# Kernel optimization log

Measured on AMD Instinct MI355X. Metric: run time of the kernel, lower is better.

The kernel has to match this reference:

```python
import jax, jax.numpy as jnp
import numpy as np
from jax import lax

N, B, H, E = 50, 1024, 256, 256
FEA, SF = 8, 5
C_TANH = 10.0  # tanh_exploration, use_tanh=True for pointer


def setup_inputs() -> dict:
    key = jax.random.key(0)
    ks = iter(jax.random.split(key, 40))
    def rn(shape):
        return jax.random.normal(next(ks), shape, dtype=jnp.float32)
    def up(shape):
        s = 1.0 / np.sqrt(shape[-1])
        return jax.random.uniform(next(ks), shape, minval=-s, maxval=s, dtype=jnp.float32)
    inp = {
        'start_fea': rn((B, SF)),
        'decoder_input': rn((B, E)),
        'embedded_inputs': rn((N, B, E)),
        'hidden_h': rn((B, H)),
        'hidden_c': rn((B, H)),
        'context': rn((N, B, H)),
        'V': rn((B, N, FEA)),
        'V_reach_mask': jnp.zeros((B, N), dtype=bool),
        # LSTMCell (pointer decoder)
        'lstm_w_ih': up((4 * H, E)), 'lstm_w_hh': up((4 * H, H)),
        'lstm_b_ih': up((4 * H,)), 'lstm_b_hh': up((4 * H,)),
        # pointer attention
        'ptr_wq': up((H, H)), 'ptr_bq': up((H,)),
        'ptr_wr': up((H, H)), 'ptr_br': up((H,)), 'ptr_v': up((H,)),
        # glimpse attention
        'glp_wq': up((H, H)), 'glp_bq': up((H,)),
        'glp_wr': up((H, H)), 'glp_br': up((H,)), 'glp_v': up((H,)),
        # eta branch
        'fn_w': up((H, SF)),
        'eta_w_ih': up((4 * H, H)), 'eta_w_hh': up((4 * H, H)),
        'eta_b_ih': up((4 * H,)), 'eta_b_hh': up((4 * H,)),
        'eta_lin_w': up((1, 2 * H)), 'eta_lin_b': up((1,)),
    }
    return inp


def _lstm_cell(x, h, c, wi, wh, bi, bh):
    z = x @ wi.T + bi + h @ wh.T + bh
    i, f, g, o = jnp.split(z, 4, axis=1)  # torch chunk order i,f,g,o
    c2 = jax.nn.sigmoid(f) * c + jax.nn.sigmoid(i) * jnp.tanh(g)
    return jax.nn.sigmoid(o) * jnp.tanh(c2), c2


def _mask_modify(m):
    # if a row is all True, un-mask its last column
    return m.at[:, -1].set(jnp.where(m.all(axis=1), False, m[:, -1]))


def reference(start_fea, decoder_input, embedded_inputs, hidden_h, hidden_c,
              context, V, V_reach_mask,
              lstm_w_ih, lstm_w_hh, lstm_b_ih, lstm_b_hh,
              ptr_wq, ptr_bq, ptr_wr, ptr_br, ptr_v,
              glp_wq, glp_bq, glp_wr, glp_br, glp_v,
              fn_w, eta_w_ih, eta_w_hh, eta_b_ih, eta_b_hh,
              eta_lin_w, eta_lin_b):
    n_steps, bsz = embedded_inputs.shape[0], embedded_inputs.shape[1]
    barange = jnp.arange(bsz)
    # project_ref is a 1x1 conv over fixed context -> precompute once: [B,H,N]
    e_ptr = jnp.einsum('nbh,gh->bgn', context, ptr_wr) + ptr_br[None, :, None]
    e_glp = jnp.einsum('nbh,gh->bgn', context, glp_wr) + glp_br[None, :, None]

    def attn_logits(q_in, e, wq, bq, v):
        q = q_in @ wq.T + bq  # [B,H]
        return jnp.einsum('h,bhn->bn', v, jnp.tanh(q[:, :, None] + e))

    first_node = start_fea @ fn_w.T  # [B,H], no bias
    he, ce = _lstm_cell(first_node, hidden_h, hidden_c, eta_w_ih, eta_w_hh, eta_b_ih, eta_b_hh)
    mask0 = _mask_modify(V_reach_mask)

    def step(carry, step_i):
        h, c, mask, idxs, dec_in, heh, cec, last_node, cur_eta = carry
        upd = _mask_modify(mask.at[barange, idxs].set(True))
        logit_mask = jnp.where(step_i == 0, mask, upd)
        # pointer LSTM step
        h, c = _lstm_cell(dec_in, h, c, lstm_w_ih, lstm_w_hh, lstm_b_ih, lstm_b_hh)
        g_l = h
        # one glimpse (n_glimpses=1, mask_glimpses=True, use_tanh=False)
        u = attn_logits(g_l, e_glp, glp_wq, glp_bq, glp_v)
        u = jnp.where(logit_mask, -jnp.inf, u)
        g_l = jnp.einsum('bhn,bn->bh', e_glp, jax.nn.softmax(u, axis=1))
        # pointer (use_tanh=True, C=10, mask_logits=True)
        u = attn_logits(g_l, e_ptr, ptr_wq, ptr_bq, ptr_v)
        logits = jnp.where(logit_mask, -jnp.inf, C_TANH * jnp.tanh(u))
        log_p = jax.nn.log_softmax(logits, axis=1)  # [B,N]
        new_idxs = jnp.argmax(log_p, axis=1)  # greedy decode
        # eta branch
        cur_node = context[new_idxs, barange]  # [B,H]
        heh, cec = _lstm_cell(cur_node, heh, cec, eta_w_ih, eta_w_hh, eta_b_ih, eta_b_hh)
        eta = jnp.concatenate([last_node, cur_node], axis=1) @ eta_lin_w.T + eta_lin_b  # [B,1]
        cur_eta = cur_eta + eta
        dec_in2 = embedded_inputs[new_idxs, barange]  # [B,E]
        new_carry = (h, c, logit_mask, new_idxs, dec_in2, heh, cec, cur_node, cur_eta)
        return new_carry, (log_p, new_idxs, cur_eta[:, 0])

    init = (hidden_h, hidden_c, mask0, jnp.zeros((bsz,), jnp.int32), decoder_input,
            he, ce, first_node, jnp.zeros((bsz, 1), jnp.float32))
    _, (log_ps, sels, etas) = lax.scan(step, init, jnp.arange(n_steps))
    # stack along step dim -> [B, N, ...]
    return log_ps.transpose(1, 0, 2), sels.T, etas.T
```

## Files before the change

kernel.cpp:

```cpp
#include <hip/hip_runtime.h>
#include <hip/hip_bf16.h>

#define NSTEP 50
#define BSZ   1024
#define HD    256
#define RPB   2
#define NEG_INF (-__builtin_inff())

#define OFF_SEL ((size_t)BSZ * NSTEP * NSTEP)
#define OFF_ETA (OFF_SEL + (size_t)BSZ * NSTEP)

__device__ __forceinline__ float sigf(float x)      { return 1.f / (1.f + __expf(-x)); }
__device__ __forceinline__ float tanh_fast(float x) { return 1.f - 2.f / (__expf(2.f * x) + 1.f); }

__device__ __forceinline__ float wave_sum(float v) {
#pragma unroll
  for (int o = 1; o < 64; o <<= 1) v += __shfl_xor(v, o);
  return v;
}
__device__ __forceinline__ float wave_max(float v) {
#pragma unroll
  for (int o = 1; o < 64; o <<= 1) v = fmaxf(v, __shfl_xor(v, o));
  return v;
}

__global__ __launch_bounds__(256) void init_kernel(
    const float* __restrict__ w_ih, const float* __restrict__ w_hh,
    const float* __restrict__ b_ih, const float* __restrict__ b_hh,
    const float* __restrict__ glp_wq, const float* __restrict__ ptr_wq,
    float* __restrict__ wT2, float* __restrict__ bc,
    float* __restrict__ wqTg, float* __restrict__ wqTp)
{
  const int bid = blockIdx.x, tid = threadIdx.x;
  if (bid < 512) {
    const int k = bid;
    const float* src = (k < 256) ? (w_ih + k) : (w_hh + (k - 256));
#pragma unroll
    for (int g = 0; g < 4; ++g)
      wT2[(size_t)k * 1024 + tid * 4 + g] = src[(size_t)(g * 256 + tid) * 256];
  } else if (bid < 516) {
    const int j = (bid - 512) * 256 + tid;
    bc[j] = b_ih[j] + b_hh[j];
  } else {
    const int k = bid - 516;
    wqTg[(size_t)k * 256 + tid] = glp_wq[(size_t)tid * 256 + k];
    wqTp[(size_t)k * 256 + tid] = ptr_wq[(size_t)tid * 256 + k];
  }
}

__global__ __launch_bounds__(256) void e_kernel(
    const float* __restrict__ context,
    const float* __restrict__ glp_wr, const float* __restrict__ glp_br,
    const float* __restrict__ ptr_wr, const float* __restrict__ ptr_br,
    float* __restrict__ e_glp, float* __restrict__ e_ptr)
{
  __shared__ float ctx_lds[32][256];
  const int tid = threadIdx.x;
  const int n   = blockIdx.x >> 5;
  const int b0  = (blockIdx.x & 31) << 5;
  const float* src = context + ((size_t)n * BSZ + b0) * HD;
  for (int i = tid; i < 32 * 64; i += 256) {
    const int row = i >> 6, k4 = (i & 63) << 2;
    *(float4*)&ctx_lds[row][k4] = *(const float4*)&src[row * HD + k4];
  }
  __syncthreads();
  const int g  = tid;
  const float bg = glp_br[g], bp = ptr_br[g];
  for (int rg = 0; rg < 2; ++rg) {
    float ag[16], ap[16];
#pragma unroll
    for (int i = 0; i < 16; ++i) { ag[i] = 0.f; ap[i] = 0.f; }
    for (int k = 0; k < 256; k += 4) {
      float4 wg = *(const float4*)&glp_wr[g * HD + k];
      float4 wp = *(const float4*)&ptr_wr[g * HD + k];
#pragma unroll
      for (int i = 0; i < 16; ++i) {
        float4 a = *(const float4*)&ctx_lds[rg * 16 + i][k];
        ag[i] += a.x * wg.x + a.y * wg.y + a.z * wg.z + a.w * wg.w;
        ap[i] += a.x * wp.x + a.y * wp.y + a.z * wp.z + a.w * wp.w;
      }
    }
#pragma unroll
    for (int i = 0; i < 16; ++i) {
      const int b = b0 + rg * 16 + i;
      e_glp[((size_t)b * NSTEP + n) * HD + g] = ag[i] + bg;
      e_ptr[((size_t)b * NSTEP + n) * HD + g] = ap[i] + bp;
    }
  }
}

__global__ __launch_bounds__(256) void zx_kernel(
    const float* __restrict__ embedded, const float* __restrict__ decoder_input,
    const float* __restrict__ wT2, float* __restrict__ zx)
{
  __shared__ float x_lds[32][256];
  const int tid = threadIdx.x;
  const int n   = blockIdx.x >> 5;
  const int b0  = (blockIdx.x & 31) << 5;
  const float* src = (n < NSTEP) ? (embedded + ((size_t)n * BSZ + b0) * HD)
                                 : (decoder_input + (size_t)b0 * HD);
  for (int i = tid; i < 32 * 64; i += 256) {
    const int row = i >> 6, k4 = (i & 63) << 2;
    *(float4*)&x_lds[row][k4] = *(const float4*)&src[row * HD + k4];
  }
  __syncthreads();
  const float* wp = wT2 + (tid << 2);
  for (int rg = 0; rg < 2; ++rg) {
    float4 acc[16];
#pragma unroll
    for (int i = 0; i < 16; ++i) acc[i] = make_float4(0.f, 0.f, 0.f, 0.f);
    for (int k = 0; k < 256; k += 4) {
      float4 w0 = *(const float4*)(wp + (size_t)(k + 0) * 1024);
      float4 w1 = *(const float4*)(wp + (size_t)(k + 1) * 1024);
      float4 w2 = *(const float4*)(wp + (size_t)(k + 2) * 1024);
      float4 w3 = *(const float4*)(wp + (size_t)(k + 3) * 1024);
#pragma unroll
      for (int i = 0; i < 16; ++i) {
        float4 a = *(const float4*)&x_lds[rg * 16 + i][k];
        acc[i].x += a.x * w0.x + a.y * w1.x + a.z * w2.x + a.w * w3.x;
        acc[i].y += a.x * w0.y + a.y * w1.y + a.z * w2.y + a.w * w3.y;
        acc[i].z += a.x * w0.z + a.y * w1.z + a.z * w2.z + a.w * w3.z;
        acc[i].w += a.x * w0.w + a.y * w1.w + a.z * w2.w + a.w * w3.w;
      }
    }
#pragma unroll
    for (int i = 0; i < 16; ++i)
      *(float4*)&zx[((size_t)n * BSZ + (b0 + rg * 16 + i)) * 1024 + (tid << 2)] = acc[i];
  }
}

template <int PRE>
__global__ __launch_bounds__(512, 4) void dec_kernel(
    const float* __restrict__ start_fea,
    const float* __restrict__ decoder_input,
    const float* __restrict__ embedded,
    const float* __restrict__ hidden_h,
    const float* __restrict__ hidden_c,
    const float* __restrict__ context,
    const unsigned char* __restrict__ vmask,
    const float* __restrict__ glp_bq, const float* __restrict__ glp_v,
    const float* __restrict__ ptr_bq, const float* __restrict__ ptr_v,
    const float* __restrict__ fn_w,
    const float* __restrict__ eta_lw, const float* __restrict__ eta_lb,
    const float* __restrict__ wT2, const float* __restrict__ bc,
    const float* __restrict__ wqTg, const float* __restrict__ wqTp,
    const float* __restrict__ e_glp, const float* __restrict__ e_ptr,
    const float* __restrict__ zx,
    float* __restrict__ out)
{
  __shared__ float a_lds[RPB][512];
  __shared__ float z_lds[RPB][1024];
  __shared__ float q_lds[RPB][512];
  __shared__ float u_lds[RPB][52];
  __shared__ unsigned char mask_lds[RPB][64];
  __shared__ float ms_lds[RPB][4][2];
  __shared__ int   idx_lds[RPB];
  __shared__ float red_lds[8];
  __shared__ float eta_lds[RPB];

  const int tid  = threadIdx.x;
  const int col  = tid & 255;
  const int hf   = tid >> 8;
  const int wav  = tid >> 6;
  const int lane = tid & 63;
  const int b0   = blockIdx.x * RPB;
  const int cr   = wav >> 2;
  const int cq   = wav & 3;
  const int n0   = cq * 13;
  const int n1   = (cq == 3) ? NSTEP : (n0 + 13);
  const int k0   = hf << 7;
  const int j2   = tid * 2;

  float c_reg, ln_reg;

  {
    const int r = hf, b = b0 + r;
    a_lds[r][256 + col] = hidden_h[(size_t)b * HD + col];
    if (!PRE) a_lds[r][col] = decoder_input[(size_t)b * HD + col];
    c_reg = hidden_c[(size_t)b * HD + col];
    float fn = 0.f;
#pragma unroll
    for (int k = 0; k < 5; ++k) fn += start_fea[b * 5 + k] * fn_w[col * 5 + k];
    ln_reg = fn;
  }
  if (tid < RPB * NSTEP) {
    const int r = tid / NSTEP, n = tid - r * NSTEP;
    mask_lds[r][n] = vmask[(size_t)(b0 + r) * NSTEP + n];
  }
  if (tid < RPB) { eta_lds[tid] = 0.f; idx_lds[tid] = NSTEP; }
  __syncthreads();
  if (tid < RPB) {
    bool all = true;
    for (int n = 0; n < NSTEP; ++n) all = all && (mask_lds[tid][n] != 0);
    if (all) mask_lds[tid][NSTEP - 1] = 0;
  }
  __syncthreads();

  const float bch0 = bc[col], bch1 = bc[col + 256], bch2 = bc[col + 512], bch3 = bc[col + 768];
  const float lw0 = eta_lw[col], lw1 = eta_lw[HD + col];
  const float etaB = eta_lb[0];
  const float4 v4g  = *(const float4*)&glp_v[lane << 2];
  const float4 v4p  = *(const float4*)&ptr_v[lane << 2];
  const float4 v4bg = *(const float4*)&glp_bq[lane << 2];
  const float4 v4bp = *(const float4*)&ptr_bq[lane << 2];

  for (int t = 0; t < NSTEP; ++t) {
    {
      float2 acc[RPB];
      if (PRE) {
#pragma unroll
        for (int i = 0; i < RPB; ++i)
          acc[i] = *(const float2*)&zx[((size_t)idx_lds[i] * BSZ + (b0 + i)) * 1024 + j2];
      } else {
#pragma unroll
        for (int i = 0; i < RPB; ++i) acc[i] = make_float2(0.f, 0.f);
      }
      const int K0 = PRE ? 256 : 0;
      for (int k = K0; k < 512; k += 4) {
        float4 a4[RPB];
#pragma unroll
        for (int i = 0; i < RPB; ++i) a4[i] = *(const float4*)&a_lds[i][k];
        const float2 w0 = *(const float2*)&wT2[(size_t)(k + 0) * 1024 + j2];
        const float2 w1 = *(const float2*)&wT2[(size_t)(k + 1) * 1024 + j2];
        const float2 w2 = *(const float2*)&wT2[(size_t)(k + 2) * 1024 + j2];
        const float2 w3 = *(const float2*)&wT2[(size_t)(k + 3) * 1024 + j2];
#pragma unroll
        for (int i = 0; i < RPB; ++i) {
          acc[i].x += a4[i].x * w0.x + a4[i].y * w1.x + a4[i].z * w2.x + a4[i].w * w3.x;
          acc[i].y += a4[i].x * w0.y + a4[i].y * w1.y + a4[i].z * w2.y + a4[i].w * w3.y;
        }
      }
#pragma unroll
      for (int i = 0; i < RPB; ++i) *(float2*)&z_lds[i][j2] = acc[i];
    }
    __syncthreads();
    {
      const float4 z4 = *(const float4*)&z_lds[hf][col << 2];
      const float zi = z4.x + bch0, zf = z4.y + bch1, zg = z4.z + bch2, zo = z4.w + bch3;
      const float cn = sigf(zf) * c_reg + sigf(zi) * tanh_fast(zg);
      c_reg = cn;
      a_lds[hf][256 + col] = sigf(zo) * tanh_fast(cn);
    }
    __syncthreads();
    {
      float accB[RPB] = {0.f, 0.f};
      for (int k = k0; k < k0 + 128; k += 4) {
        float4 a4[RPB];
#pragma unroll
        for (int i = 0; i < RPB; ++i) a4[i] = *(const float4*)&a_lds[i][256 + k];
        const float w0 = wqTg[(size_t)(k + 0) * 256 + col];
        const float w1 = wqTg[(size_t)(k + 1) * 256 + col];
        const float w2 = wqTg[(size_t)(k + 2) * 256 + col];
        const float w3 = wqTg[(size_t)(k + 3) * 256 + col];
#pragma unroll
        for (int i = 0; i < RPB; ++i)
          accB[i] += a4[i].x * w0 + a4[i].y * w1 + a4[i].z * w2 + a4[i].w * w3;
      }
#pragma unroll
      for (int i = 0; i < RPB; ++i) q_lds[i][(hf << 8) + col] = accB[i];
    }
    __syncthreads();
    {
      const int r = cr, b = b0 + r;
      float4 q4;
      {
        const float4 p0 = *(const float4*)&q_lds[r][lane << 2];
        const float4 p1 = *(const float4*)&q_lds[r][256 + (lane << 2)];
        q4 = make_float4(p0.x + p1.x + v4bg.x, p0.y + p1.y + v4bg.y,
                         p0.z + p1.z + v4bg.z, p0.w + p1.w + v4bg.w);
      }
      float m = NEG_INF, s = 0.f;
      float4 G = make_float4(0.f, 0.f, 0.f, 0.f);
      const float* eb = e_glp + (size_t)b * NSTEP * HD;
      for (int n = n0; n < n1; ++n) {
        if (mask_lds[r][n]) continue;
        const float4 e4 = *(const float4*)&eb[n * HD + (lane << 2)];
        float uu = v4g.x * tanh_fast(q4.x + e4.x) + v4g.y * tanh_fast(q4.y + e4.y)
                 + v4g.z * tanh_fast(q4.z + e4.z) + v4g.w * tanh_fast(q4.w + e4.w);
        uu = wave_sum(uu);
        if (uu > m) {
          const float sc = __expf(m - uu);
          s *= sc; G.x *= sc; G.y *= sc; G.z *= sc; G.w *= sc;
          m = uu;
        }
        const float p = __expf(uu - m);
        s += p;
        G.x += p * e4.x; G.y += p * e4.y; G.z += p * e4.z; G.w += p * e4.w;
      }
      if (lane == 0) { ms_lds[r][cq][0] = m; ms_lds[r][cq][1] = s; }
      __syncthreads();
      float mg = NEG_INF;
#pragma unroll
      for (int q = 0; q < 4; ++q) mg = fmaxf(mg, ms_lds[r][q][0]);
      float Z = 0.f;
#pragma unroll
      for (int q = 0; q < 4; ++q) Z += ms_lds[r][q][1] * __expf(ms_lds[r][q][0] - mg);
      const float sc = __expf(m - mg) / Z;
      G.x *= sc; G.y *= sc; G.z *= sc; G.w *= sc;
      *(float4*)&z_lds[r][(cq << 8) + (lane << 2)] = G;
    }
    __syncthreads();
    {
      float accE[RPB] = {0.f, 0.f};
      for (int k = k0; k < k0 + 128; k += 4) {
        float4 g4[RPB];
#pragma unroll
        for (int i = 0; i < RPB; ++i) {
          const float4 g0 = *(const float4*)&z_lds[i][k];
          const float4 g1 = *(const float4*)&z_lds[i][256 + k];
          const float4 g2 = *(const float4*)&z_lds[i][512 + k];
          const float4 g3 = *(const float4*)&z_lds[i][768 + k];
          g4[i] = make_float4(g0.x + g1.x + g2.x + g3.x, g0.y + g1.y + g2.y + g3.y,
                              g0.z + g1.z + g2.z + g3.z, g0.w + g1.w + g2.w + g3.w);
        }
        const float w0 = wqTp[(size_t)(k + 0) * 256 + col];
        const float w1 = wqTp[(size_t)(k + 1) * 256 + col];
        const float w2 = wqTp[(size_t)(k + 2) * 256 + col];
        const float w3 = wqTp[(size_t)(k + 3) * 256 + col];
#pragma unroll
        for (int i = 0; i < RPB; ++i)
          accE[i] += g4[i].x * w0 + g4[i].y * w1 + g4[i].z * w2 + g4[i].w * w3;
      }
#pragma unroll
      for (int i = 0; i < RPB; ++i) q_lds[i][(hf << 8) + col] = accE[i];
    }
    __syncthreads();
    {
      const int r = cr, b = b0 + r;
      float4 q4;
      {
        const float4 p0 = *(const float4*)&q_lds[r][lane << 2];
        const float4 p1 = *(const float4*)&q_lds[r][256 + (lane << 2)];
        q4 = make_float4(p0.x + p1.x + v4bp.x, p0.y + p1.y + v4bp.y,
                         p0.z + p1.z + v4bp.z, p0.w + p1.w + v4bp.w);
      }
      const float* eb = e_ptr + (size_t)b * NSTEP * HD;
      for (int n = n0; n < n1; ++n) {
        const float4 e4 = *(const float4*)&eb[n * HD + (lane << 2)];
        float uu = v4p.x * tanh_fast(q4.x + e4.x) + v4p.y * tanh_fast(q4.y + e4.y)
                 + v4p.z * tanh_fast(q4.z + e4.z) + v4p.w * tanh_fast(q4.w + e4.w);
        uu = wave_sum(uu);
        if (lane == 0) u_lds[r][n] = uu;
      }
    }
    __syncthreads();
    if (wav < RPB) {
      const int r = wav, b = b0 + r;
      const bool mk = (lane < NSTEP) ? (mask_lds[r][lane] != 0) : true;
      const float lg = mk ? NEG_INF : (10.f * tanh_fast(u_lds[r][lane]));
      const float m  = wave_max(lg);
      const float ex = (lane < NSTEP) ? __expf(lg - m) : 0.f;
      const float ss = wave_sum(ex);
      const float ls = __logf(ss);
      if (lane < NSTEP)
        out[(size_t)b * (NSTEP * NSTEP) + (size_t)t * NSTEP + lane] =
            mk ? -1.0e30f : ((lg - m) - ls);
      float av = lg;
      int   ai = lane;
#pragma unroll
      for (int o = 1; o < 64; o <<= 1) {
        const float ov = __shfl_xor(av, o);
        const int   oi = __shfl_xor(ai, o);
        if (ov > av || (ov == av && oi < ai)) { av = ov; ai = oi; }
      }
      if (lane == 0) {
        idx_lds[r] = ai;
        out[OFF_SEL + (size_t)b * NSTEP + t] = (float)ai;
      }
    }
    __syncthreads();
    {
      const int r = hf, b = b0 + r;
      const int ix = idx_lds[r];
      const float cur = context[((size_t)ix * BSZ + b) * HD + col];
      float pr = ln_reg * lw0 + cur * lw1;
      ln_reg = cur;
      if (!PRE) a_lds[r][col] = embedded[((size_t)ix * BSZ + b) * HD + col];
      pr = wave_sum(pr);
      if (lane == 0) red_lds[wav] = pr;
    }
    __syncthreads();
    if (tid < RPB) {
      const int r = tid;
      const float s = red_lds[r * 4 + 0] + red_lds[r * 4 + 1]
                    + red_lds[r * 4 + 2] + red_lds[r * 4 + 3];
      const float ev = eta_lds[r] + s + etaB;
      eta_lds[r] = ev;
      out[OFF_ETA + (size_t)(b0 + r) * NSTEP + t] = ev;
      const int ix = idx_lds[r];
      mask_lds[r][ix] = 1;
      bool all = true;
      for (int n = 0; n < NSTEP; ++n) all = all && (mask_lds[r][n] != 0);
      if (all) mask_lds[r][NSTEP - 1] = 0;
    }
    __syncthreads();
  }
}

extern "C" void kernel_launch(void* const* d_in, const int* in_sizes, int n_in,
                              void* d_out, int out_size, void* d_ws, size_t ws_size,
                              hipStream_t stream) {
  const float* start_fea  = (const float*)d_in[0];
  const float* decoder_in = (const float*)d_in[1];
  const float* embedded   = (const float*)d_in[2];
  const float* hidden_h   = (const float*)d_in[3];
  const float* hidden_c   = (const float*)d_in[4];
  const float* context    = (const float*)d_in[5];
  const unsigned char* vmask = (const unsigned char*)d_in[7];
  const float* lstm_w_ih  = (const float*)d_in[8];
  const float* lstm_w_hh  = (const float*)d_in[9];
  const float* lstm_b_ih  = (const float*)d_in[10];
  const float* lstm_b_hh  = (const float*)d_in[11];
  const float* ptr_wq     = (const float*)d_in[12];
  const float* ptr_bq     = (const float*)d_in[13];
  const float* ptr_wr     = (const float*)d_in[14];
  const float* ptr_br     = (const float*)d_in[15];
  const float* ptr_v      = (const float*)d_in[16];
  const float* glp_wq     = (const float*)d_in[17];
  const float* glp_bq     = (const float*)d_in[18];
  const float* glp_wr     = (const float*)d_in[19];
  const float* glp_br     = (const float*)d_in[20];
  const float* glp_v      = (const float*)d_in[21];
  const float* fn_w       = (const float*)d_in[22];
  const float* eta_lw     = (const float*)d_in[27];
  const float* eta_lb     = (const float*)d_in[28];

  float* ws    = (float*)d_ws;
  float* e_glp = ws;
  float* e_ptr = e_glp + (size_t)BSZ * NSTEP * HD;
  float* wT2   = e_ptr + (size_t)BSZ * NSTEP * HD;
  float* bc    = wT2 + (size_t)512 * 1024;
  float* wqTg  = bc + 1024;
  float* wqTp  = wqTg + 65536;
  float* zx    = wqTp + 65536;

  const size_t need_pre =
      ((size_t)BSZ * NSTEP * HD * 2 + (size_t)512 * 1024 + 1024 + 2 * 65536 +
       (size_t)(NSTEP + 1) * BSZ * 1024) * sizeof(float);
  const bool pre = (ws_size >= need_pre);

  init_kernel<<<772, 256, 0, stream>>>(lstm_w_ih, lstm_w_hh, lstm_b_ih, lstm_b_hh,
                                       glp_wq, ptr_wq, wT2, bc, wqTg, wqTp);
  e_kernel<<<NSTEP * 32, 256, 0, stream>>>(context, glp_wr, glp_br, ptr_wr, ptr_br, e_glp, e_ptr);
  if (pre) {
    zx_kernel<<<(NSTEP + 1) * 32, 256, 0, stream>>>(embedded, decoder_in, wT2, zx);
    dec_kernel<1><<<BSZ / RPB, 512, 0, stream>>>(
        start_fea, decoder_in, embedded, hidden_h, hidden_c, context, vmask,
        glp_bq, glp_v, ptr_bq, ptr_v, fn_w, eta_lw, eta_lb,
        wT2, bc, wqTg, wqTp, e_glp, e_ptr, zx, (float*)d_out);
  } else {
    dec_kernel<0><<<BSZ / RPB, 512, 0, stream>>>(
        start_fea, decoder_in, embedded, hidden_h, hidden_c, context, vmask,
        glp_bq, glp_v, ptr_bq, ptr_v, fn_w, eta_lw, eta_lb,
        wT2, bc, wqTg, wqTp, e_glp, e_ptr, zx, (float*)d_out);
  }
}
```

Measured before the change: 5.995 ms.

## Process four batch rows per 1024-thread block to halve weight re-reads

Doubles rows per block from 2 to 4 and block size from 512 to 1024 threads. Each thread now owns one gate column, and the query projections split K four ways, so every weight load from global memory serves four batch rows. The goal is to cut the L2/HBM traffic from re-streaming the LSTM and query weights on each step. It also skips masked nodes in the pointer attention loop. The cost is fewer blocks (256), an extra reduction pass through LDS with more barriers, and lower occupancy from dropping the launch-bounds hint.

```diff
diff --git a/kernel.cpp b/kernel.cpp
--- a/kernel.cpp
+++ b/kernel.cpp
@@ -4,7 +4,7 @@
 #define NSTEP 50
 #define BSZ   1024
 #define HD    256
-#define RPB   2
+#define RPB   4
 #define NEG_INF (-__builtin_inff())
 
 #define OFF_SEL ((size_t)BSZ * NSTEP * NSTEP)
@@ -130,7 +130,7 @@
 }
 
 template <int PRE>
-__global__ __launch_bounds__(512, 4) void dec_kernel(
+__global__ __launch_bounds__(1024) void dec_kernel(
     const float* __restrict__ start_fea,
     const float* __restrict__ decoder_input,
     const float* __restrict__ embedded,
@@ -150,17 +150,18 @@
 {
   __shared__ float a_lds[RPB][512];
   __shared__ float z_lds[RPB][1024];
-  __shared__ float q_lds[RPB][512];
+  __shared__ float z2_lds[RPB][1024];
+  __shared__ float qf_lds[RPB][256];
   __shared__ float u_lds[RPB][52];
   __shared__ unsigned char mask_lds[RPB][64];
   __shared__ float ms_lds[RPB][4][2];
   __shared__ int   idx_lds[RPB];
-  __shared__ float red_lds[8];
+  __shared__ float red_lds[16];
   __shared__ float eta_lds[RPB];
 
   const int tid  = threadIdx.x;
   const int col  = tid & 255;
-  const int hf   = tid >> 8;
+  const int rr   = tid >> 8;
   const int wav  = tid >> 6;
   const int lane = tid & 63;
   const int b0   = blockIdx.x * RPB;
@@ -168,15 +169,14 @@
   const int cq   = wav & 3;
   const int n0   = cq * 13;
   const int n1   = (cq == 3) ? NSTEP : (n0 + 13);
-  const int k0   = hf << 7;
-  const int j2   = tid * 2;
+  const int kq   = rr;
 
   float c_reg, ln_reg;
 
   {
-    const int r = hf, b = b0 + r;
-    a_lds[r][256 + col] = hidden_h[(size_t)b * HD + col];
-    if (!PRE) a_lds[r][col] = decoder_input[(size_t)b * HD + col];
+    const int b = b0 + rr;
+    a_lds[rr][256 + col] = hidden_h[(size_t)b * HD + col];
+    if (!PRE) a_lds[rr][col] = decoder_input[(size_t)b * HD + col];
     c_reg = hidden_c[(size_t)b * HD + col];
     float fn = 0.f;
 #pragma unroll
@@ -199,76 +199,81 @@
   const float bch0 = bc[col], bch1 = bc[col + 256], bch2 = bc[col + 512], bch3 = bc[col + 768];
   const float lw0 = eta_lw[col], lw1 = eta_lw[HD + col];
   const float etaB = eta_lb[0];
-  const float4 v4g  = *(const float4*)&glp_v[lane << 2];
-  const float4 v4p  = *(const float4*)&ptr_v[lane << 2];
-  const float4 v4bg = *(const float4*)&glp_bq[lane << 2];
-  const float4 v4bp = *(const float4*)&ptr_bq[lane << 2];
+  const float bqg = glp_bq[col], bqp = ptr_bq[col];
+  const float4 v4g = *(const float4*)&glp_v[lane << 2];
+  const float4 v4p = *(const float4*)&ptr_v[lane << 2];
 
   for (int t = 0; t < NSTEP; ++t) {
     {
-      float2 acc[RPB];
+      float acc[RPB];
       if (PRE) {
 #pragma unroll
         for (int i = 0; i < RPB; ++i)
-          acc[i] = *(const float2*)&zx[((size_t)idx_lds[i] * BSZ + (b0 + i)) * 1024 + j2];
+          acc[i] = zx[((size_t)idx_lds[i] * BSZ + (b0 + i)) * 1024 + tid];
+        const float* wp = wT2 + (size_t)256 * 1024 + tid;
+        for (int k = 0; k < 256; k += 4) {
+          const float w0 = wp[(size_t)(k + 0) * 1024];
+          const float w1 = wp[(size_t)(k + 1) * 1024];
+          const float w2 = wp[(size_t)(k + 2) * 1024];
+          const float w3 = wp[(size_t)(k + 3) * 1024];
+#pragma unroll
+          for (int i = 0; i < RPB; ++i) {
+            const float4 a4 = *(const float4*)&a_lds[i][256 + k];
+            acc[i] += a4.x * w0 + a4.y * w1 + a4.z * w2 + a4.w * w3;
+          }
+        }
       } else {
 #pragma unroll
-        for (int i = 0; i < RPB; ++i) acc[i] = make_float2(0.f, 0.f);
-      }
-      const int K0 = PRE ? 256 : 0;
-      for (int k = K0; k < 512; k += 4) {
-        float4 a4[RPB];
-#pragma unroll
-        for (int i = 0; i < RPB; ++i) a4[i] = *(const float4*)&a_lds[i][k];
-        const float2 w0 = *(const float2*)&wT2[(size_t)(k + 0) * 1024 + j2];
-        const float2 w1 = *(const float2*)&wT2[(size_t)(k + 1) * 1024 + j2];
-        const float2 w2 = *(const float2*)&wT2[(size_t)(k + 2) * 1024 + j2];
-        const float2 w3 = *(const float2*)&wT2[(size_t)(k + 3) * 1024 + j2];
-#pragma unroll
-        for (int i = 0; i < RPB; ++i) {
-          acc[i].x += a4[i].x * w0.x + a4[i].y * w1.x + a4[i].z * w2.x + a4[i].w * w3.x;
-          acc[i].y += a4[i].x * w0.y + a4[i].y * w1.y + a4[i].z * w2.y + a4[i].w * w3.y;
+        for (int i = 0; i < RPB; ++i) acc[i] = 0.f;
+        const float* wp = wT2 + tid;
+        for (int k = 0; k < 512; k += 4) {
+          const float w0 = wp[(size_t)(k + 0) * 1024];
+          const float w1 = wp[(size_t)(k + 1) * 1024];
+          const float w2 = wp[(size_t)(k + 2) * 1024];
+          const float w3 = wp[(size_t)(k + 3) * 1024];
+#pragma unroll
+          for (int i = 0; i < RPB; ++i) {
+            const float4 a4 = *(const float4*)&a_lds[i][k];
+            acc[i] += a4.x * w0 + a4.y * w1 + a4.z * w2 + a4.w * w3;
+          }
         }
       }
 #pragma unroll
-      for (int i = 0; i < RPB; ++i) *(float2*)&z_lds[i][j2] = acc[i];
-    }
-    __syncthreads();
-    {
-      const float4 z4 = *(const float4*)&z_lds[hf][col << 2];
+      for (int i = 0; i < RPB; ++i) z_lds[i][tid] = acc[i];
+    }
+    __syncthreads();
+    {
+      const float4 z4 = *(const float4*)&z_lds[rr][col << 2];
       const float zi = z4.x + bch0, zf = z4.y + bch1, zg = z4.z + bch2, zo = z4.w + bch3;
       const float cn = sigf(zf) * c_reg + sigf(zi) * tanh_fast(zg);
       c_reg = cn;
-      a_lds[hf][256 + col] = sigf(zo) * tanh_fast(cn);
-    }
-    __syncthreads();
-    {
-      float accB[RPB] = {0.f, 0.f};
-      for (int k = k0; k < k0 + 128; k += 4) {
-        float4 a4[RPB];
-#pragma unroll
-        for (int i = 0; i < RPB; ++i) a4[i] = *(const float4*)&a_lds[i][256 + k];
+      a_lds[rr][256 + col] = sigf(zo) * tanh_fast(cn);
+    }
+    __syncthreads();
+    {
+      float accB[RPB] = {0.f, 0.f, 0.f, 0.f};
+      const int kb = kq << 6;
+      for (int k = kb; k < kb + 64; k += 4) {
         const float w0 = wqTg[(size_t)(k + 0) * 256 + col];
         const float w1 = wqTg[(size_t)(k + 1) * 256 + col];
         const float w2 = wqTg[(size_t)(k + 2) * 256 + col];
         const float w3 = wqTg[(size_t)(k + 3) * 256 + col];
 #pragma unroll
-        for (int i = 0; i < RPB; ++i)
-          accB[i] += a4[i].x * w0 + a4[i].y * w1 + a4[i].z * w2 + a4[i].w * w3;
-      }
-#pragma unroll
-      for (int i = 0; i < RPB; ++i) q_lds[i][(hf << 8) + col] = accB[i];
-    }
+        for (int i = 0; i < RPB; ++i) {
+          const float4 a4 = *(const float4*)&a_lds[i][256 + k];
+          accB[i] += a4.x * w0 + a4.y * w1 + a4.z * w2 + a4.w * w3;
+        }
+      }
+#pragma unroll
+      for (int i = 0; i < RPB; ++i) z_lds[i][(kq << 8) + col] = accB[i];
+    }
+    __syncthreads();
+    qf_lds[rr][col] = z_lds[rr][col] + z_lds[rr][256 + col]
+                    + z_lds[rr][512 + col] + z_lds[rr][768 + col] + bqg;
     __syncthreads();
     {
       const int r = cr, b = b0 + r;
-      float4 q4;
-      {
-        const float4 p0 = *(const float4*)&q_lds[r][lane << 2];
-        const float4 p1 = *(const float4*)&q_lds[r][256 + (lane << 2)];
-        q4 = make_float4(p0.x + p1.x + v4bg.x, p0.y + p1.y + v4bg.y,
-                         p0.z + p1.z + v4bg.z, p0.w + p1.w + v4bg.w);
-      }
+      const float4 q4 = *(const float4*)&qf_lds[r][lane << 2];
       float m = NEG_INF, s = 0.f;
       float4 G = make_float4(0.f, 0.f, 0.f, 0.f);
       const float* eb = e_glp + (size_t)b * NSTEP * HD;
@@ -297,45 +302,43 @@
       for (int q = 0; q < 4; ++q) Z += ms_lds[r][q][1] * __expf(ms_lds[r][q][0] - mg);
       const float sc = __expf(m - mg) / Z;
       G.x *= sc; G.y *= sc; G.z *= sc; G.w *= sc;
-      *(float4*)&z_lds[r][(cq << 8) + (lane << 2)] = G;
-    }
-    __syncthreads();
-    {
-      float accE[RPB] = {0.f, 0.f};
-      for (int k = k0; k < k0 + 128; k += 4) {
-        float4 g4[RPB];
-#pragma unroll
-        for (int i = 0; i < RPB; ++i) {
-          const float4 g0 = *(const float4*)&z_lds[i][k];
-          const float4 g1 = *(const float4*)&z_lds[i][256 + k];
-          const float4 g2 = *(const float4*)&z_lds[i][512 + k];
-          const float4 g3 = *(const float4*)&z_lds[i][768 + k];
-          g4[i] = make_float4(g0.x + g1.x + g2.x + g3.x, g0.y + g1.y + g2.y + g3.y,
-                              g0.z + g1.z + g2.z + g3.z, g0.w + g1.w + g2.w + g3.w);
-        }
+      *(float4*)&z2_lds[r][(cq << 8) + (lane << 2)] = G;
+    }
+    __syncthreads();
+    {
+      float accE[RPB] = {0.f, 0.f, 0.f, 0.f};
+      const int kb = kq << 6;
+      for (int k = kb; k < kb + 64; k += 4) {
         const float w0 = wqTp[(size_t)(k + 0) * 256 + col];
         const float w1 = wqTp[(size_t)(k + 1) * 256 + col];
         const float w2 = wqTp[(size_t)(k + 2) * 256 + col];
         const float w3 = wqTp[(size_t)(k + 3) * 256 + col];
 #pragma unroll
-        for (int i = 0; i < RPB; ++i)
-          accE[i] += g4[i].x * w0 + g4[i].y * w1 + g4[i].z * w2 + g4[i].w * w3;
-      }
-#pragma unroll
-      for (int i = 0; i < RPB; ++i) q_lds[i][(hf << 8) + col] = accE[i];
-    }
+        for (int i = 0; i < RPB; ++i) {
+          const float4 g0 = *(const float4*)&z2_lds[i][k];
+          const float4 g1 = *(const float4*)&z2_lds[i][256 + k];
+          const float4 g2 = *(const float4*)&z2_lds[i][512 + k];
+          const float4 g3 = *(const float4*)&z2_lds[i][768 + k];
+          const float gx = g0.x + g1.x + g2.x + g3.x;
+          const float gy = g0.y + g1.y + g2.y + g3.y;
+          const float gz = g0.z + g1.z + g2.z + g3.z;
+          const float gw = g0.w + g1.w + g2.w + g3.w;
+          accE[i] += gx * w0 + gy * w1 + gz * w2 + gw * w3;
+        }
+      }
+#pragma unroll
+      for (int i = 0; i < RPB; ++i) z_lds[i][(kq << 8) + col] = accE[i];
+    }
+    __syncthreads();
+    qf_lds[rr][col] = z_lds[rr][col] + z_lds[rr][256 + col]
+                    + z_lds[rr][512 + col] + z_lds[rr][768 + col] + bqp;
     __syncthreads();
     {
       const int r = cr, b = b0 + r;
-      float4 q4;
-      {
-        const float4 p0 = *(const float4*)&q_lds[r][lane << 2];
-        const float4 p1 = *(const float4*)&q_lds[r][256 + (lane << 2)];
-        q4 = make_float4(p0.x + p1.x + v4bp.x, p0.y + p1.y + v4bp.y,
-                         p0.z + p1.z + v4bp.z, p0.w + p1.w + v4bp.w);
-      }
+      const float4 q4 = *(const float4*)&qf_lds[r][lane << 2];
       const float* eb = e_ptr + (size_t)b * NSTEP * HD;
       for (int n = n0; n < n1; ++n) {
+        if (mask_lds[r][n]) continue;
         const float4 e4 = *(const float4*)&eb[n * HD + (lane << 2)];
         float uu = v4p.x * tanh_fast(q4.x + e4.x) + v4p.y * tanh_fast(q4.y + e4.y)
                  + v4p.z * tanh_fast(q4.z + e4.z) + v4p.w * tanh_fast(q4.w + e4.w);
@@ -349,7 +352,7 @@
       const bool mk = (lane < NSTEP) ? (mask_lds[r][lane] != 0) : true;
       const float lg = mk ? NEG_INF : (10.f * tanh_fast(u_lds[r][lane]));
       const float m  = wave_max(lg);
-      const float ex = (lane < NSTEP) ? __expf(lg - m) : 0.f;
+      const float ex = mk ? 0.f : __expf(lg - m);
       const float ss = wave_sum(ex);
       const float ls = __logf(ss);
       if (lane < NSTEP)
@@ -370,12 +373,12 @@
     }
     __syncthreads();
     {
-      const int r = hf, b = b0 + r;
-      const int ix = idx_lds[r];
+      const int b = b0 + rr;
+      const int ix = idx_lds[rr];
       const float cur = context[((size_t)ix * BSZ + b) * HD + col];
       float pr = ln_reg * lw0 + cur * lw1;
       ln_reg = cur;
-      if (!PRE) a_lds[r][col] = embedded[((size_t)ix * BSZ + b) * HD + col];
+      if (!PRE) a_lds[rr][col] = embedded[((size_t)ix * BSZ + b) * HD + col];
       pr = wave_sum(pr);
       if (lane == 0) red_lds[wav] = pr;
     }
@@ -444,12 +447,12 @@
   e_kernel<<<NSTEP * 32, 256, 0, stream>>>(context, glp_wr, glp_br, ptr_wr, ptr_br, e_glp, e_ptr);
   if (pre) {
     zx_kernel<<<(NSTEP + 1) * 32, 256, 0, stream>>>(embedded, decoder_in, wT2, zx);
-    dec_kernel<1><<<BSZ / RPB, 512, 0, stream>>>(
+    dec_kernel<1><<<BSZ / RPB, 1024, 0, stream>>>(
         start_fea, decoder_in, embedded, hidden_h, hidden_c, context, vmask,
         glp_bq, glp_v, ptr_bq, ptr_v, fn_w, eta_lw, eta_lb,
         wT2, bc, wqTg, wqTp, e_glp, e_ptr, zx, (float*)d_out);
   } else {
-    dec_kernel<0><<<BSZ / RPB, 512, 0, stream>>>(
+    dec_kernel<0><<<BSZ / RPB, 1024, 0, stream>>>(
         start_fea, decoder_in, embedded, hidden_h, hidden_c, context, vmask,
         glp_bq, glp_v, ptr_bq, ptr_v, fn_w, eta_lw, eta_lb,
         wT2, bc, wqTg, wqTp, e_glp, e_ptr, zx, (float*)d_out);
```

Measured after the change: 5.095 ms. 1.18x faster.
